# Kernel tuning notes

Measured on AMD Instinct MI355X. Metric: run time of the kernel, lower is better.

## Reference

```python
import jax, jax.numpy as jnp
import numpy as np

L, B, T, D, H, F, V = 8, 2, 1024, 1024, 16, 4096, 50257


def _ln(x, w, b):
    m = jnp.mean(x, axis=-1, keepdims=True)
    v = jnp.mean((x - m) ** 2, axis=-1, keepdims=True)
    return (x - m) * jax.lax.rsqrt(v + 1e-5) * w + b


def setup_inputs() -> dict:
    key = jax.random.key(0)
    ks = iter(jax.random.split(key, 16))
    s = jnp.float32(0.02)
    w = lambda shape: jax.random.normal(next(ks), shape, jnp.float32) * s
    return {
        'idx': jax.random.randint(next(ks), (B, T), 0, V, jnp.int32),
        'emb': w((V, D)),
        'pos_emb': w((T, D)),
        'ln1_w': jnp.ones((L, D), jnp.float32),
        'ln1_b': jnp.zeros((L, D), jnp.float32),
        'qkv_w': w((L, D, 3 * D)),
        'qkv_b': jnp.zeros((L, 3 * D), jnp.float32),
        'ln2_w': jnp.ones((L, D), jnp.float32),
        'ln2_b': jnp.zeros((L, D), jnp.float32),
        'fc1_w': w((L, D, F)),
        'fc1_b': jnp.zeros((L, F), jnp.float32),
        'fc2_w': w((L, F, D)),
        'fc2_b': jnp.zeros((L, D), jnp.float32),
        'lnf_w': jnp.ones((D,), jnp.float32),
        'lnf_b': jnp.zeros((D,), jnp.float32),
        'head_w': w((D, V)),
        'head_b': jnp.zeros((V,), jnp.float32),
    }


def reference(idx, emb, pos_emb, ln1_w, ln1_b, qkv_w, qkv_b, ln2_w, ln2_b,
              fc1_w, fc1_b, fc2_w, fc2_b, lnf_w, lnf_b, head_w, head_b):
    b, t = idx.shape
    d = emb.shape[1]
    hd = d // H
    x = emb[idx] + pos_emb[:t]                      # [b,t,d]
    mask = jnp.tril(jnp.ones((t, t), bool))         # causal mask
    inv_scale = jnp.float32(1.0 / (d ** 0.5))       # NOTE: source scales by sqrt(full dim), not head_dim

    def layer(x, p):
        l1w, l1b, qw, qb, l2w, l2b, f1w, f1b, f2w, f2b = p
        h = _ln(x, l1w, l1b)
        qkv = h @ qw + qb                           # [b,t,3d]
        q, k, v = jnp.split(qkv, 3, axis=-1)
        q = q.reshape(b, t, H, hd)
        k = k.reshape(b, t, H, hd)
        v = v.reshape(b, t, H, hd)
        logits = jnp.einsum('bqhe,bkhe->bhqk', q, k) * inv_scale
        logits = jnp.where(mask, logits, -jnp.inf)
        attn = jax.nn.softmax(logits, axis=-1)
        o = jnp.einsum('bhqk,bkhe->bqhe', attn, v).reshape(b, t, d)
        x = x + o                                   # no output projection in source
        h = _ln(x, l2w, l2b)
        h = jax.nn.gelu(h @ f1w + f1b, approximate=False)
        h = jax.nn.gelu(h @ f2w + f2b, approximate=False)  # GELU after fc2 too, per source
        return x + h, None

    x, _ = jax.lax.scan(
        layer, x,
        (ln1_w, ln1_b, qkv_w, qkv_b, ln2_w, ln2_b, fc1_w, fc1_b, fc2_w, fc2_b))
    x = _ln(x, lnf_w, lnf_b)
    return x @ head_w + head_b                      # [b,t,V] logits
```

## Files before the change

### kernel.cpp

```cpp
#include <hip/hip_runtime.h>
#include <math.h>

#define Ln 8
#define Bn 2
#define Tn 1024
#define Dm 1024
#define Hn 16
#define Fm 4096
#define Vn 50257
#define NTOK 2048

typedef unsigned short u16;
typedef u16   u16x8  __attribute__((ext_vector_type(8)));
typedef __bf16 bf16x8 __attribute__((ext_vector_type(8)));
typedef float f32x4  __attribute__((ext_vector_type(4)));

__device__ __forceinline__ u16 f2bf(float f){
  unsigned u = __builtin_bit_cast(unsigned, f);
  u += 0x7FFFu + ((u >> 16) & 1u);
  return (u16)(u >> 16);
}
__device__ __forceinline__ float bf2f(u16 s){
  return __builtin_bit_cast(float, ((unsigned)s) << 16);
}
__device__ __forceinline__ float gelu_f(float v){
  return 0.5f * v * (1.0f + erff(v * 0.70710678118654752440f));
}
__device__ __forceinline__ void gload16(const void* g, void* l){
  __builtin_amdgcn_global_load_lds(
      (const __attribute__((address_space(1))) void*)g,
      (__attribute__((address_space(3))) void*)l, 16, 0, 0);
}

__global__ __launch_bounds__(256) void embed_kernel(const int* __restrict__ idx,
                                                    const float* __restrict__ emb,
                                                    const float* __restrict__ pos,
                                                    float* __restrict__ x){
  int row = blockIdx.x;
  int t = row & (Tn - 1);
  int id = idx[row];
  const float4* e = (const float4*)(emb + (size_t)id * Dm);
  const float4* p = (const float4*)(pos + (size_t)t * Dm);
  float4* o = (float4*)(x + (size_t)row * Dm);
  int i = threadIdx.x;
  float4 a = e[i], b = p[i];
  o[i] = make_float4(a.x + b.x, a.y + b.y, a.z + b.z, a.w + b.w);
}

__global__ __launch_bounds__(256) void ln_kernel(const float* __restrict__ xin,
                                                 const float* __restrict__ w,
                                                 const float* __restrict__ bb,
                                                 u16* __restrict__ out){
  int row = blockIdx.x;
  int t = threadIdx.x;
  float4 v = ((const float4*)(xin + (size_t)row * Dm))[t];
  float s  = v.x + v.y + v.z + v.w;
  float s2 = v.x*v.x + v.y*v.y + v.z*v.z + v.w*v.w;
  #pragma unroll
  for (int off = 1; off < 64; off <<= 1){
    s  += __shfl_xor(s, off);
    s2 += __shfl_xor(s2, off);
  }
  __shared__ float red[8];
  int wv = t >> 6, lane = t & 63;
  if (lane == 0){ red[wv] = s; red[4 + wv] = s2; }
  __syncthreads();
  s  = red[0] + red[1] + red[2] + red[3];
  s2 = red[4] + red[5] + red[6] + red[7];
  float mean = s * (1.0f / Dm);
  float var  = s2 * (1.0f / Dm) - mean * mean;
  float rs = rsqrtf(var + 1e-5f);
  float4 wv4 = ((const float4*)w)[t];
  float4 bv4 = ((const float4*)bb)[t];
  u16 o4[4];
  o4[0] = f2bf((v.x - mean) * rs * wv4.x + bv4.x);
  o4[1] = f2bf((v.y - mean) * rs * wv4.y + bv4.y);
  o4[2] = f2bf((v.z - mean) * rs * wv4.z + bv4.z);
  o4[3] = f2bf((v.w - mean) * rs * wv4.w + bv4.w);
  *(uint2*)(out + (size_t)row * Dm + t * 4) = *(uint2*)o4;
}

__global__ __launch_bounds__(256) void transpose_w(const float* __restrict__ Bw,
                                                   u16* __restrict__ Bt,
                                                   int N, int K, int c0){
  int n0 = blockIdx.x * 64, k0 = blockIdx.y * 64;
  __shared__ float tile[64][66];
  int t = threadIdx.x;
  int rr = t >> 4, nc = (t & 15) * 4;
  #pragma unroll
  for (int u = 0; u < 4; u++){
    int kk = rr + u * 16;
    int gn = c0 + n0 + nc;
    const float* src = Bw + (size_t)(k0 + kk) * N;
    float4 v;
    if (gn + 3 < N) v = *(const float4*)(src + gn);
    else {
      v.x = (gn     < N) ? src[gn]     : 0.0f;
      v.y = (gn + 1 < N) ? src[gn + 1] : 0.0f;
      v.z = (gn + 2 < N) ? src[gn + 2] : 0.0f;
      v.w = (gn + 3 < N) ? src[gn + 3] : 0.0f;
    }
    tile[kk][nc]     = v.x;
    tile[kk][nc + 1] = v.y;
    tile[kk][nc + 2] = v.z;
    tile[kk][nc + 3] = v.w;
  }
  __syncthreads();
  int np = t >> 2, c = t & 3;
  u16* dst = Bt + (size_t)(n0 + np) * K + k0;
  u16 pk[8];
  #pragma unroll
  for (int j = 0; j < 8; j++) pk[j] = f2bf(tile[c*8 + j][np]);
  *(int4*)(dst + c*8) = *(int4*)pk;
  #pragma unroll
  for (int j = 0; j < 8; j++) pk[j] = f2bf(tile[32 + c*8 + j][np]);
  *(int4*)(dst + 32 + c*8) = *(int4*)pk;
}

#define BM 128
#define BN 128
template<int MODE>
__global__ __launch_bounds__(256) void gemm_kernel(const u16* __restrict__ A,
                                                   const u16* __restrict__ Bt,
                                                   const float* __restrict__ bias,
                                                   void* __restrict__ outp,
                                                   float* __restrict__ resid,
                                                   u16* __restrict__ vT,
                                                   int K, int Nout, int c0){
  __shared__ u16 sA[128][64];
  __shared__ u16 sB[128][64];
  int t = threadIdx.x;
  int lane = t & 63, w = t >> 6;
  int wm = w >> 1, wn = w & 1;
  int lr = lane & 15, lg = lane >> 4;
  int m0 = blockIdx.y * BM, n0 = blockIdx.x * BN;

  f32x4 acc[4][4] = {};

  int srow = lane >> 3, scol = (lane & 7) * 8;
  int cswz = ((lr >> 2) & 3) << 4;

  for (int k0 = 0; k0 < K; k0 += 64){
    __syncthreads();
    #pragma unroll
    for (int i = 0; i < 4; i++){
      int rbase = i*32 + w*8;
      int r = rbase + srow;
      int gc = scol ^ (((r >> 2) & 3) << 4);
      gload16(A  + (size_t)(m0 + r) * K + k0 + gc, (char*)&sA[rbase][0]);
      gload16(Bt + (size_t)(n0 + r) * K + k0 + gc, (char*)&sB[rbase][0]);
    }
    __syncthreads();
    #pragma unroll
    for (int kk = 0; kk < 2; kk++){
      bf16x8 af[4], bfr[4];
      #pragma unroll
      for (int i = 0; i < 4; i++) af[i]  = *(const bf16x8*)&sA[wm*64 + i*16 + lr][(kk*32 + lg*8) ^ cswz];
      #pragma unroll
      for (int j = 0; j < 4; j++) bfr[j] = *(const bf16x8*)&sB[wn*64 + j*16 + lr][(kk*32 + lg*8) ^ cswz];
      #pragma unroll
      for (int i = 0; i < 4; i++)
        #pragma unroll
        for (int j = 0; j < 4; j++)
          acc[i][j] = __builtin_amdgcn_mfma_f32_16x16x32_bf16(af[i], bfr[j], acc[i][j], 0, 0, 0);
    }
  }

  #pragma unroll
  for (int i = 0; i < 4; i++){
    int gr0 = m0 + wm*64 + i*16 + lg*4;
    #pragma unroll
    for (int j = 0; j < 4; j++){
      int gc = c0 + n0 + wn*64 + j*16 + lr;
      if (MODE == 3 && gc >= Nout) continue;
      float bb = bias[gc];
      if (MODE == 0 && gc >= 2048){
        int hh = (gc - 2048) >> 6, dd = (gc - 2048) & 63;
        int b_ = gr0 >> 10, tt = gr0 & 1023;
        u16 pk[4];
        #pragma unroll
        for (int r = 0; r < 4; r++) pk[r] = f2bf(acc[i][j][r] + bb);
        *(uint2*)&vT[((size_t)((b_*Hn + hh)*64 + dd))*Tn + tt] = *(uint2*)pk;
        continue;
      }
      #pragma unroll
      for (int r = 0; r < 4; r++){
        float v = acc[i][j][r] + bb;
        size_t oi = (size_t)(gr0 + r) * Nout + gc;
        if (MODE == 0)      ((u16*)outp)[oi] = f2bf(v);
        else if (MODE == 1) ((u16*)outp)[oi] = f2bf(gelu_f(v));
        else if (MODE == 2) resid[oi] = resid[oi] + gelu_f(v);
        else                ((float*)outp)[oi] = v;
      }
    }
  }
}

__global__ __launch_bounds__(256) void attn_mfma(const u16* __restrict__ qkv,
                                                 const u16* __restrict__ vT,
                                                 float* __restrict__ x){
  int bid = blockIdx.x;
  int bh = bid & 31;
  int j = bid >> 5;
  int qt = (j < 8) ? (15 - j) : (j - 8);
  int b = bh >> 4, h_ = bh & 15;
  int t = threadIdx.x;
  int w = t >> 6, lane = t & 63;
  int lr = lane & 15, lg = lane >> 4;

  __shared__ u16 sK [2][64][72];
  __shared__ u16 sVt[2][64][72];
  __shared__ u16 sP [64][72];

  const u16* qbase = qkv + ((size_t)(b*Tn + qt*64 + w*16 + lr)) * 3*Dm + h_*64 + lg*8;
  bf16x8 qf[2];
  #pragma unroll
  for (int i = 0; i < 2; i++){
    u16x8 raw = *(const u16x8*)(qbase + i * 32);
    #pragma unroll
    for (int u = 0; u < 8; u++) qf[i][u] = (__bf16)(bf2f(raw[u]) * 0.03125f);
  }

  f32x4 o_[4] = {};
  float m_[4], l_[4];
  #pragma unroll
  for (int r = 0; r < 4; r++){ m_[r] = -INFINITY; l_[r] = 0.0f; }

  int sr = t >> 2, scc = (t & 3) * 16;
  const u16* kbase = qkv + ((size_t)(b*Tn + sr)) * 3*Dm + Dm + h_*64 + scc;
  const u16* vbase = vT + ((size_t)(bh*64 + sr)) * Tn + scc;
  int4 kr0, kr1, vr0, vr1;

  kr0 = *(const int4*)(kbase);     kr1 = *(const int4*)(kbase + 8);
  vr0 = *(const int4*)(vbase);     vr1 = *(const int4*)(vbase + 8);
  *(int4*)&sK [0][sr][scc]     = kr0;  *(int4*)&sK [0][sr][scc + 8] = kr1;
  *(int4*)&sVt[0][sr][scc]     = vr0;  *(int4*)&sVt[0][sr][scc + 8] = vr1;

  for (int kt = 0; kt <= qt; kt++){
    int cur = kt & 1;
    if (kt < qt){
      const u16* kb = kbase + (size_t)(kt + 1) * 64 * 3 * Dm;
      const u16* vb = vbase + (kt + 1) * 64;
      kr0 = *(const int4*)(kb);    kr1 = *(const int4*)(kb + 8);
      vr0 = *(const int4*)(vb);    vr1 = *(const int4*)(vb + 8);
    }
    __syncthreads();

    f32x4 s[4] = {};
    __builtin_amdgcn_s_setprio(1);
    #pragma unroll
    for (int kf = 0; kf < 2; kf++){
      #pragma unroll
      for (int nf = 0; nf < 4; nf++){
        bf16x8 kfrag = *(const bf16x8*)&sK[cur][nf*16 + lr][kf*32 + lg*8];
        s[nf] = __builtin_amdgcn_mfma_f32_16x16x32_bf16(qf[kf], kfrag, s[nf], 0, 0, 0);
      }
    }
    __builtin_amdgcn_s_setprio(0);

    bool lastt = (kt == qt);
    float tmax[4] = {-INFINITY, -INFINITY, -INFINITY, -INFINITY};
    #pragma unroll
    for (int nf = 0; nf < 4; nf++)
      #pragma unroll
      for (int r = 0; r < 4; r++){
        float v = s[nf][r];
        if (lastt){
          int kkg = nf*16 + lr, qg = w*16 + lg*4 + r;
          if (kkg > qg) v = -INFINITY;
        }
        s[nf][r] = v;
        tmax[r] = fmaxf(tmax[r], v);
      }
    #pragma unroll
    for (int r = 0; r < 4; r++){
      tmax[r] = fmaxf(tmax[r], __shfl_xor(tmax[r], 1));
      tmax[r] = fmaxf(tmax[r], __shfl_xor(tmax[r], 2));
      tmax[r] = fmaxf(tmax[r], __shfl_xor(tmax[r], 4));
      tmax[r] = fmaxf(tmax[r], __shfl_xor(tmax[r], 8));
    }
    float resc[4], psum[4];
    #pragma unroll
    for (int r = 0; r < 4; r++){
      float nm = fmaxf(m_[r], tmax[r]);
      resc[r] = __expf(m_[r] - nm);
      m_[r] = nm;
      psum[r] = 0.0f;
    }
    #pragma unroll
    for (int nf = 0; nf < 4; nf++)
      #pragma unroll
      for (int r = 0; r < 4; r++){
        float pv = __expf(s[nf][r] - m_[r]);
        s[nf][r] = pv;
        psum[r] += pv;
      }
    #pragma unroll
    for (int r = 0; r < 4; r++){
      psum[r] += __shfl_xor(psum[r], 1);
      psum[r] += __shfl_xor(psum[r], 2);
      psum[r] += __shfl_xor(psum[r], 4);
      psum[r] += __shfl_xor(psum[r], 8);
      l_[r] = l_[r] * resc[r] + psum[r];
    }
    #pragma unroll
    for (int df = 0; df < 4; df++)
      #pragma unroll
      for (int r = 0; r < 4; r++)
        o_[df][r] *= resc[r];

    #pragma unroll
    for (int nf = 0; nf < 4; nf++)
      #pragma unroll
      for (int r = 0; r < 4; r++)
        sP[w*16 + lg*4 + r][nf*16 + lr] = f2bf(s[nf][r]);

    __builtin_amdgcn_s_setprio(1);
    #pragma unroll
    for (int kf = 0; kf < 2; kf++){
      bf16x8 pfrag = *(const bf16x8*)&sP[w*16 + lr][kf*32 + lg*8];
      #pragma unroll
      for (int df = 0; df < 4; df++){
        bf16x8 vfrag = *(const bf16x8*)&sVt[cur][df*16 + lr][kf*32 + lg*8];
        o_[df] = __builtin_amdgcn_mfma_f32_16x16x32_bf16(pfrag, vfrag, o_[df], 0, 0, 0);
      }
    }
    __builtin_amdgcn_s_setprio(0);

    if (kt < qt){
      int nxt = cur ^ 1;
      *(int4*)&sK [nxt][sr][scc]     = kr0;  *(int4*)&sK [nxt][sr][scc + 8] = kr1;
      *(int4*)&sVt[nxt][sr][scc]     = vr0;  *(int4*)&sVt[nxt][sr][scc + 8] = vr1;
    }
  }

  float inv[4];
  #pragma unroll
  for (int r = 0; r < 4; r++) inv[r] = 1.0f / l_[r];
  #pragma unroll
  for (int df = 0; df < 4; df++)
    #pragma unroll
    for (int r = 0; r < 4; r++){
      float* xr = x + ((size_t)(b*Tn + qt*64 + w*16 + lg*4 + r)) * Dm + h_*64 + df*16 + lr;
      *xr += o_[df][r] * inv[r];
    }
}

extern "C" void kernel_launch(void* const* d_in, const int* in_sizes, int n_in,
                              void* d_out, int out_size, void* d_ws, size_t ws_size,
                              hipStream_t stream){
  const int*   idx   = (const int*)  d_in[0];
  const float* emb   = (const float*)d_in[1];
  const float* pos   = (const float*)d_in[2];
  const float* ln1w  = (const float*)d_in[3];
  const float* ln1b  = (const float*)d_in[4];
  const float* qkvw  = (const float*)d_in[5];
  const float* qkvb  = (const float*)d_in[6];
  const float* ln2w  = (const float*)d_in[7];
  const float* ln2b  = (const float*)d_in[8];
  const float* fc1w  = (const float*)d_in[9];
  const float* fc1b  = (const float*)d_in[10];
  const float* fc2w  = (const float*)d_in[11];
  const float* fc2b  = (const float*)d_in[12];
  const float* lnfw  = (const float*)d_in[13];
  const float* lnfb  = (const float*)d_in[14];
  const float* headw = (const float*)d_in[15];
  const float* headb = (const float*)d_in[16];
  float* out = (float*)d_out;

  char* ws = (char*)d_ws;
  float* x   = (float*)(ws);
  u16*   h   = (u16*)  (ws + (8u  << 20));
  u16*   qkv = (u16*)  (ws + (12u << 20));
  u16*   f1  = (u16*)  (ws + (24u << 20));
  u16*   Bt  = (u16*)  (ws + (40u << 20));
  u16*   vT  = (u16*)  (ws + (48u << 20));
  u16*   BtF = (u16*)  (ws + (12u << 20));

  embed_kernel<<<NTOK, 256, 0, stream>>>(idx, emb, pos, x);

  for (int l = 0; l < Ln; l++){
    ln_kernel<<<NTOK, 256, 0, stream>>>(x, ln1w + l*Dm, ln1b + l*Dm, h);
    transpose_w<<<dim3(3072/64, Dm/64), 256, 0, stream>>>(qkvw + (size_t)l*Dm*3072, Bt, 3072, Dm, 0);
    gemm_kernel<0><<<dim3(3072/BN, NTOK/BM), 256, 0, stream>>>(h, Bt, qkvb + l*3072, qkv, nullptr, vT, Dm, 3072, 0);
    attn_mfma<<<512, 256, 0, stream>>>(qkv, vT, x);
    ln_kernel<<<NTOK, 256, 0, stream>>>(x, ln2w + l*Dm, ln2b + l*Dm, h);
    transpose_w<<<dim3(Fm/64, Dm/64), 256, 0, stream>>>(fc1w + (size_t)l*Dm*Fm, Bt, Fm, Dm, 0);
    gemm_kernel<1><<<dim3(Fm/BN, NTOK/BM), 256, 0, stream>>>(h, Bt, fc1b + l*Fm, f1, nullptr, nullptr, Dm, Fm, 0);
    transpose_w<<<dim3(Dm/64, Fm/64), 256, 0, stream>>>(fc2w + (size_t)l*Fm*Dm, Bt, Dm, Fm, 0);
    gemm_kernel<2><<<dim3(Dm/BN, NTOK/BM), 256, 0, stream>>>(f1, Bt, fc2b + l*Dm, nullptr, x, nullptr, Fm, Dm, 0);
  }

  ln_kernel<<<NTOK, 256, 0, stream>>>(x, lnfw, lnfb, h);

  if (ws_size >= (116u << 20)){
    transpose_w<<<dim3(786, Dm/64), 256, 0, stream>>>(headw, BtF, Vn, Dm, 0);
    gemm_kernel<3><<<dim3(393, NTOK/BM), 256, 0, stream>>>(h, BtF, headb, out, nullptr, nullptr, Dm, Vn, 0);
  } else {
    const int CHUNK = 4096;
    for (int c0 = 0; c0 < Vn; c0 += CHUNK){
      int W = Vn - c0; if (W > CHUNK) W = CHUNK;
      int ngx = (W + BN - 1) / BN;
      transpose_w<<<dim3(ngx * 2, Dm/64), 256, 0, stream>>>(headw, Bt, Vn, Dm, c0);
      gemm_kernel<3><<<dim3(ngx, NTOK/BM), 256, 0, stream>>>(h, Bt, headb, out, nullptr, nullptr, Dm, Vn, c0);
    }
  }
}
```

Baseline: 2.000 ms.

## Batch all weight transposes up front, retile GEMMs, swizzle head GEMM blocks

Adds a single mega_transpose launch that converts all layer and head weights to bf16 transposed layout once at the start, when the workspace is large enough, removing per-layer transpose launches. Templates the GEMM on tile shape and warp layout, using 64x128 tiles for the qkv and fc2 GEMMs to produce more blocks. Adds a block-index swizzle for the vocab head GEMM to improve L2 locality across XCDs. The mega path needs over 320MB of workspace and falls back otherwise.

Measured after the change: 1.916 ms. -4.2%, faster.

```diff
diff --git a/kernel.cpp b/kernel.cpp
--- a/kernel.cpp
+++ b/kernel.cpp
@@ -80,46 +80,86 @@
   *(uint2*)(out + (size_t)row * Dm + t * 4) = *(uint2*)o4;
 }
 
+__device__ __forceinline__ void trans_tile(const float* __restrict__ src,
+                                           u16* __restrict__ dst,
+                                           int N, int K, int srcCol, int dstRow, int k0){
+  __shared__ float tile[64][66];
+  int t = threadIdx.x;
+  int rr = t >> 4, nc = (t & 15) * 4;
+  #pragma unroll
+  for (int u = 0; u < 4; u++){
+    int kk = rr + u * 16;
+    int gn = srcCol + nc;
+    const float* sp = src + (size_t)(k0 + kk) * N;
+    float4 v;
+    if (gn + 3 < N) v = *(const float4*)(sp + gn);
+    else {
+      v.x = (gn     < N) ? sp[gn]     : 0.0f;
+      v.y = (gn + 1 < N) ? sp[gn + 1] : 0.0f;
+      v.z = (gn + 2 < N) ? sp[gn + 2] : 0.0f;
+      v.w = (gn + 3 < N) ? sp[gn + 3] : 0.0f;
+    }
+    tile[kk][nc]     = v.x;
+    tile[kk][nc + 1] = v.y;
+    tile[kk][nc + 2] = v.z;
+    tile[kk][nc + 3] = v.w;
+  }
+  __syncthreads();
+  int np = t >> 2, c = t & 3;
+  u16* dp = dst + (size_t)(dstRow + np) * K + k0;
+  u16 pk[8];
+  #pragma unroll
+  for (int j = 0; j < 8; j++) pk[j] = f2bf(tile[c*8 + j][np]);
+  *(int4*)(dp + c*8) = *(int4*)pk;
+  #pragma unroll
+  for (int j = 0; j < 8; j++) pk[j] = f2bf(tile[32 + c*8 + j][np]);
+  *(int4*)(dp + 32 + c*8) = *(int4*)pk;
+}
+
 __global__ __launch_bounds__(256) void transpose_w(const float* __restrict__ Bw,
                                                    u16* __restrict__ Bt,
                                                    int N, int K, int c0){
   int n0 = blockIdx.x * 64, k0 = blockIdx.y * 64;
-  __shared__ float tile[64][66];
-  int t = threadIdx.x;
-  int rr = t >> 4, nc = (t & 15) * 4;
-  #pragma unroll
-  for (int u = 0; u < 4; u++){
-    int kk = rr + u * 16;
-    int gn = c0 + n0 + nc;
-    const float* src = Bw + (size_t)(k0 + kk) * N;
-    float4 v;
-    if (gn + 3 < N) v = *(const float4*)(src + gn);
-    else {
-      v.x = (gn     < N) ? src[gn]     : 0.0f;
-      v.y = (gn + 1 < N) ? src[gn + 1] : 0.0f;
-      v.z = (gn + 2 < N) ? src[gn + 2] : 0.0f;
-      v.w = (gn + 3 < N) ? src[gn + 3] : 0.0f;
-    }
-    tile[kk][nc]     = v.x;
-    tile[kk][nc + 1] = v.y;
-    tile[kk][nc + 2] = v.z;
-    tile[kk][nc + 3] = v.w;
-  }
-  __syncthreads();
-  int np = t >> 2, c = t & 3;
-  u16* dst = Bt + (size_t)(n0 + np) * K + k0;
-  u16 pk[8];
-  #pragma unroll
-  for (int j = 0; j < 8; j++) pk[j] = f2bf(tile[c*8 + j][np]);
-  *(int4*)(dst + c*8) = *(int4*)pk;
-  #pragma unroll
-  for (int j = 0; j < 8; j++) pk[j] = f2bf(tile[32 + c*8 + j][np]);
-  *(int4*)(dst + 32 + c*8) = *(int4*)pk;
-}
-
-#define BM 128
-#define BN 128
-template<int MODE>
+  trans_tile(Bw, Bt, N, K, c0 + n0, n0, k0);
+}
+
+__global__ __launch_bounds__(256) void mega_transpose(const float* __restrict__ qkvw,
+                                                      const float* __restrict__ fc1w,
+                                                      const float* __restrict__ fc2w,
+                                                      const float* __restrict__ headw,
+                                                      u16* __restrict__ Wq,
+                                                      u16* __restrict__ W1,
+                                                      u16* __restrict__ W2,
+                                                      u16* __restrict__ Wh){
+  int id = blockIdx.x;
+  const float* src; u16* dst; int N, K, n0, k0;
+  if (id < 6144){
+    int l = id / 768, r = id % 768;
+    n0 = (r % 48) * 64; k0 = (r / 48) * 64;
+    src = qkvw + (size_t)l * Dm * 3072; dst = Wq + (size_t)l * 3072 * Dm;
+    N = 3072; K = Dm;
+  } else if (id < 14336){
+    int id2 = id - 6144;
+    int l = id2 / 1024, r = id2 % 1024;
+    n0 = (r % 64) * 64; k0 = (r / 64) * 64;
+    src = fc1w + (size_t)l * Dm * Fm; dst = W1 + (size_t)l * Fm * Dm;
+    N = Fm; K = Dm;
+  } else if (id < 22528){
+    int id2 = id - 14336;
+    int l = id2 / 1024, r = id2 % 1024;
+    n0 = (r % 16) * 64; k0 = (r / 16) * 64;
+    src = fc2w + (size_t)l * Fm * Dm; dst = W2 + (size_t)l * Dm * Fm;
+    N = Dm; K = Fm;
+  } else {
+    int id2 = id - 22528;
+    n0 = (id2 % 786) * 64; k0 = (id2 / 786) * 64;
+    src = headw; dst = Wh;
+    N = Vn; K = Dm;
+  }
+  trans_tile(src, dst, N, K, n0, n0, k0);
+}
+
+template<int MODE, int BMt, int BNt, int WM, int WN, bool SWZ>
 __global__ __launch_bounds__(256) void gemm_kernel(const u16* __restrict__ A,
                                                    const u16* __restrict__ Bt,
                                                    const float* __restrict__ bias,
@@ -127,15 +167,26 @@
                                                    float* __restrict__ resid,
                                                    u16* __restrict__ vT,
                                                    int K, int Nout, int c0){
-  __shared__ u16 sA[128][64];
-  __shared__ u16 sB[128][64];
+  constexpr int MR = BMt / (WM * 16);
+  constexpr int NR = BNt / (WN * 16);
+  __shared__ u16 sA[BMt][64];
+  __shared__ u16 sB[BNt][64];
   int t = threadIdx.x;
   int lane = t & 63, w = t >> 6;
-  int wm = w >> 1, wn = w & 1;
+  int wm = w / WN, wn = w % WN;
   int lr = lane & 15, lg = lane >> 4;
-  int m0 = blockIdx.y * BM, n0 = blockIdx.x * BN;
-
-  f32x4 acc[4][4] = {};
+  int m0, n0;
+  if (SWZ){
+    int orig = blockIdx.x;
+    int q = gridDim.x >> 3;
+    int wg = (orig & 7) * q + (orig >> 3);
+    m0 = (wg & 15) * BMt;
+    n0 = (wg >> 4) * BNt;
+  } else {
+    m0 = blockIdx.y * BMt; n0 = blockIdx.x * BNt;
+  }
+
+  f32x4 acc[MR][NR] = {};
 
   int srow = lane >> 3, scol = (lane & 7) * 8;
   int cswz = ((lr >> 2) & 3) << 4;
@@ -143,35 +194,41 @@
   for (int k0 = 0; k0 < K; k0 += 64){
     __syncthreads();
     #pragma unroll
-    for (int i = 0; i < 4; i++){
+    for (int i = 0; i < BMt/32; i++){
       int rbase = i*32 + w*8;
       int r = rbase + srow;
       int gc = scol ^ (((r >> 2) & 3) << 4);
-      gload16(A  + (size_t)(m0 + r) * K + k0 + gc, (char*)&sA[rbase][0]);
+      gload16(A + (size_t)(m0 + r) * K + k0 + gc, (char*)&sA[rbase][0]);
+    }
+    #pragma unroll
+    for (int i = 0; i < BNt/32; i++){
+      int rbase = i*32 + w*8;
+      int r = rbase + srow;
+      int gc = scol ^ (((r >> 2) & 3) << 4);
       gload16(Bt + (size_t)(n0 + r) * K + k0 + gc, (char*)&sB[rbase][0]);
     }
     __syncthreads();
     #pragma unroll
     for (int kk = 0; kk < 2; kk++){
-      bf16x8 af[4], bfr[4];
-      #pragma unroll
-      for (int i = 0; i < 4; i++) af[i]  = *(const bf16x8*)&sA[wm*64 + i*16 + lr][(kk*32 + lg*8) ^ cswz];
-      #pragma unroll
-      for (int j = 0; j < 4; j++) bfr[j] = *(const bf16x8*)&sB[wn*64 + j*16 + lr][(kk*32 + lg*8) ^ cswz];
-      #pragma unroll
-      for (int i = 0; i < 4; i++)
+      bf16x8 af[MR], bfr[NR];
+      #pragma unroll
+      for (int i = 0; i < MR; i++) af[i]  = *(const bf16x8*)&sA[wm*(MR*16) + i*16 + lr][(kk*32 + lg*8) ^ cswz];
+      #pragma unroll
+      for (int j = 0; j < NR; j++) bfr[j] = *(const bf16x8*)&sB[wn*(NR*16) + j*16 + lr][(kk*32 + lg*8) ^ cswz];
+      #pragma unroll
+      for (int i = 0; i < MR; i++)
         #pragma unroll
-        for (int j = 0; j < 4; j++)
+        for (int j = 0; j < NR; j++)
           acc[i][j] = __builtin_amdgcn_mfma_f32_16x16x32_bf16(af[i], bfr[j], acc[i][j], 0, 0, 0);
     }
   }
 
   #pragma unroll
-  for (int i = 0; i < 4; i++){
-    int gr0 = m0 + wm*64 + i*16 + lg*4;
-    #pragma unroll
-    for (int j = 0; j < 4; j++){
-      int gc = c0 + n0 + wn*64 + j*16 + lr;
+  for (int i = 0; i < MR; i++){
+    int gr0 = m0 + wm*(MR*16) + i*16 + lg*4;
+    #pragma unroll
+    for (int j = 0; j < NR; j++){
+      int gc = c0 + n0 + wn*(NR*16) + j*16 + lr;
       if (MODE == 3 && gc >= Nout) continue;
       float bb = bias[gc];
       if (MODE == 0 && gc >= 2048){
@@ -368,41 +425,63 @@
   const float* headb = (const float*)d_in[16];
   float* out = (float*)d_out;
 
+  const size_t MB = 1u << 20;
   char* ws = (char*)d_ws;
   float* x   = (float*)(ws);
-  u16*   h   = (u16*)  (ws + (8u  << 20));
-  u16*   qkv = (u16*)  (ws + (12u << 20));
-  u16*   f1  = (u16*)  (ws + (24u << 20));
-  u16*   Bt  = (u16*)  (ws + (40u << 20));
-  u16*   vT  = (u16*)  (ws + (48u << 20));
-  u16*   BtF = (u16*)  (ws + (12u << 20));
+  u16*   h   = (u16*)  (ws + 8*MB);
+  u16*   qkv = (u16*)  (ws + 12*MB);
+  u16*   f1  = (u16*)  (ws + 24*MB);
+
+  bool mega    = ws_size >= 320*MB;
+  bool bighead = ws_size >= 116*MB;
+
+  u16 *vT, *Bt = nullptr, *BtF = nullptr, *Wq = nullptr, *W1 = nullptr, *W2 = nullptr, *Wh = nullptr;
+  if (mega){
+    vT = (u16*)(ws + 40*MB);
+    Wq = (u16*)(ws + 44*MB);
+    W1 = (u16*)(ws + 92*MB);
+    W2 = (u16*)(ws + 156*MB);
+    Wh = (u16*)(ws + 220*MB);
+  } else {
+    Bt  = (u16*)(ws + 40*MB);
+    vT  = (u16*)(ws + 48*MB);
+    BtF = (u16*)(ws + 12*MB);
+  }
+
+  if (mega)
+    mega_transpose<<<35104, 256, 0, stream>>>(qkvw, fc1w, fc2w, headw, Wq, W1, W2, Wh);
 
   embed_kernel<<<NTOK, 256, 0, stream>>>(idx, emb, pos, x);
 
   for (int l = 0; l < Ln; l++){
+    const u16* Bq = mega ? Wq + (size_t)l*3072*Dm : Bt;
+    const u16* B1 = mega ? W1 + (size_t)l*Fm*Dm   : Bt;
+    const u16* B2 = mega ? W2 + (size_t)l*Dm*Fm   : Bt;
     ln_kernel<<<NTOK, 256, 0, stream>>>(x, ln1w + l*Dm, ln1b + l*Dm, h);
-    transpose_w<<<dim3(3072/64, Dm/64), 256, 0, stream>>>(qkvw + (size_t)l*Dm*3072, Bt, 3072, Dm, 0);
-    gemm_kernel<0><<<dim3(3072/BN, NTOK/BM), 256, 0, stream>>>(h, Bt, qkvb + l*3072, qkv, nullptr, vT, Dm, 3072, 0);
+    if (!mega) transpose_w<<<dim3(3072/64, Dm/64), 256, 0, stream>>>(qkvw + (size_t)l*Dm*3072, Bt, 3072, Dm, 0);
+    gemm_kernel<0, 64,128,1,4,false><<<dim3(3072/128, NTOK/64), 256, 0, stream>>>(h, Bq, qkvb + l*3072, qkv, nullptr, vT, Dm, 3072, 0);
     attn_mfma<<<512, 256, 0, stream>>>(qkv, vT, x);
     ln_kernel<<<NTOK, 256, 0, stream>>>(x, ln2w + l*Dm, ln2b + l*Dm, h);
-    transpose_w<<<dim3(Fm/64, Dm/64), 256, 0, stream>>>(fc1w + (size_t)l*Dm*Fm, Bt, Fm, Dm, 0);
-    gemm_kernel<1><<<dim3(Fm/BN, NTOK/BM), 256, 0, stream>>>(h, Bt, fc1b + l*Fm, f1, nullptr, nullptr, Dm, Fm, 0);
-    transpose_w<<<dim3(Dm/64, Fm/64), 256, 0, stream>>>(fc2w + (size_t)l*Fm*Dm, Bt, Dm, Fm, 0);
-    gemm_kernel<2><<<dim3(Dm/BN, NTOK/BM), 256, 0, stream>>>(f1, Bt, fc2b + l*Dm, nullptr, x, nullptr, Fm, Dm, 0);
+    if (!mega) transpose_w<<<dim3(Fm/64, Dm/64), 256, 0, stream>>>(fc1w + (size_t)l*Dm*Fm, Bt, Fm, Dm, 0);
+    gemm_kernel<1,128,128,2,2,false><<<dim3(Fm/128, NTOK/128), 256, 0, stream>>>(h, B1, fc1b + l*Fm, f1, nullptr, nullptr, Dm, Fm, 0);
+    if (!mega) transpose_w<<<dim3(Dm/64, Fm/64), 256, 0, stream>>>(fc2w + (size_t)l*Fm*Dm, Bt, Dm, Fm, 0);
+    gemm_kernel<2, 64,128,1,4,false><<<dim3(Dm/128, NTOK/64), 256, 0, stream>>>(f1, B2, fc2b + l*Dm, nullptr, x, nullptr, Fm, Dm, 0);
   }
 
   ln_kernel<<<NTOK, 256, 0, stream>>>(x, lnfw, lnfb, h);
 
-  if (ws_size >= (116u << 20)){
+  if (mega){
+    gemm_kernel<3,128,128,2,2,true><<<6288, 256, 0, stream>>>(h, Wh, headb, out, nullptr, nullptr, Dm, Vn, 0);
+  } else if (bighead){
     transpose_w<<<dim3(786, Dm/64), 256, 0, stream>>>(headw, BtF, Vn, Dm, 0);
-    gemm_kernel<3><<<dim3(393, NTOK/BM), 256, 0, stream>>>(h, BtF, headb, out, nullptr, nullptr, Dm, Vn, 0);
+    gemm_kernel<3,128,128,2,2,true><<<6288, 256, 0, stream>>>(h, BtF, headb, out, nullptr, nullptr, Dm, Vn, 0);
   } else {
     const int CHUNK = 4096;
     for (int c0 = 0; c0 < Vn; c0 += CHUNK){
       int W = Vn - c0; if (W > CHUNK) W = CHUNK;
-      int ngx = (W + BN - 1) / BN;
+      int ngx = (W + 127) / 128;
       transpose_w<<<dim3(ngx * 2, Dm/64), 256, 0, stream>>>(headw, Bt, Vn, Dm, c0);
-      gemm_kernel<3><<<dim3(ngx, NTOK/BM), 256, 0, stream>>>(h, Bt, headb, out, nullptr, nullptr, Dm, Vn, c0);
-    }
-  }
-}
+      gemm_kernel<3,128,128,2,2,false><<<dim3(ngx, NTOK/128), 256, 0, stream>>>(h, Bt, headb, out, nullptr, nullptr, Dm, Vn, c0);
+    }
+  }
+}
```
